# Kernel tuning notes

Hardware: AMD Instinct MI355X
Metric: run time of the kernel (lower is better)

Reference implementation:

```python
import jax, jax.numpy as jnp
import numpy as np

HID = 32
R = 3
B = 2
IN = 64
N = 100000
E = 1600000
G = 256


def setup_inputs() -> dict:
    key = jax.random.key(0)
    ks = jax.random.split(key, 16)
    x = jax.random.normal(ks[0], (N, IN), dtype=jnp.float32)
    src = jax.random.randint(ks[1], (E,), 0, N)
    dst = jax.random.randint(ks[2], (E,), 0, N)
    etype = jax.random.randint(ks[3], (E,), 0, R)
    graph_ids = jnp.sort(jax.random.randint(ks[4], (N,), 0, G))
    s = 0.05
    basis1 = jax.random.normal(ks[5], (B, IN, HID), dtype=jnp.float32) * s   # layer 1 basis
    basis_r = jax.random.normal(ks[6], (3, B, HID, HID), dtype=jnp.float32) * s  # layers 2-4
    w_comp = jax.random.normal(ks[7], (4, R, B), dtype=jnp.float32) * s     # per-layer basis coeffs
    loop1 = jax.random.normal(ks[8], (IN, HID), dtype=jnp.float32) * s
    loop_r = jax.random.normal(ks[9], (3, HID, HID), dtype=jnp.float32) * s
    bias = jnp.zeros((4, HID), dtype=jnp.float32)
    lin1_w = jax.random.normal(ks[10], (4 * HID, 64), dtype=jnp.float32) * s
    lin1_b = jnp.zeros((64,), dtype=jnp.float32)
    lin2_w = jax.random.normal(ks[11], (64, 1), dtype=jnp.float32) * s
    lin2_b = jnp.zeros((1,), dtype=jnp.float32)
    return dict(x=x, basis1=basis1, basis_r=basis_r, w_comp=w_comp, loop1=loop1,
                loop_r=loop_r, bias=bias, lin1_w=lin1_w, lin1_b=lin1_b,
                lin2_w=lin2_w, lin2_b=lin2_b, src=src, dst=dst, etype=etype,
                graph_ids=graph_ids, num_graphs=G)


def _rel_conv(h, basis, comp, loop_w, b, src, dst, etype, n_nodes):
    # basis-decomposed relation weights: W[r] = sum_b comp[r,b] * basis[b]
    W = jnp.einsum('rb,bio->rio', comp, basis)            # [R, in, out]
    h_rel = jnp.einsum('ni,rio->rno', h, W)               # [R, N, out]
    msg = h_rel[etype, src]                               # [E, out] edge-typed gather
    agg = jax.ops.segment_sum(msg, dst, num_segments=n_nodes)
    return agg + h @ loop_w + b                           # self-loop + bias


def reference(x, basis1, basis_r, w_comp, loop1, loop_r, bias,
              lin1_w, lin1_b, lin2_w, lin2_b,
              src, dst, etype, graph_ids, num_graphs):
    n = x.shape[0]
    h = jnp.tanh(_rel_conv(x, basis1, w_comp[0], loop1, bias[0], src, dst, etype, n))
    states = [h]
    for i in range(3):
        h = jnp.tanh(_rel_conv(h, basis_r[i], w_comp[i + 1], loop_r[i], bias[i + 1],
                               src, dst, etype, n))
        states.append(h)
    feat = jnp.concatenate(states, axis=1)                # [N, 128]
    # mean-pool nodes per graph (diff_pooling ~ dgl mean_nodes)
    summed = jax.ops.segment_sum(feat, graph_ids, num_segments=num_graphs)
    counts = jax.ops.segment_sum(jnp.ones((n,), feat.dtype), graph_ids,
                                 num_segments=num_graphs)
    pooled = summed / jnp.maximum(counts, 1.0)[:, None]   # [G, 128]
    hdn = jax.nn.relu(pooled @ lin1_w + lin1_b)
    out = jax.nn.sigmoid(hdn @ lin2_w + lin2_b)
    return out[:, 0]
```

## Files before the change

### kernel.cpp

```cpp
#include <hip/hip_runtime.h>
#include <cstdint>
#include <cmath>

#define DLO_BITS 7
#define DLO_MASK 127
#define CHUNK 4096

__global__ __launch_bounds__(256) void prep_w(
    const float* __restrict__ basis1,
    const float* __restrict__ w_comp,
    const float* __restrict__ loop1,
    float* __restrict__ W)
{
    int tid = blockIdx.x * 256 + threadIdx.x;
    if (tid < 8192) {
        int m = tid >> 11, io = tid & 2047;
        W[tid] = (m < 3)
            ? w_comp[m * 2] * basis1[io] + w_comp[m * 2 + 1] * basis1[2048 + io]
            : loop1[io];
    }
}

__global__ __launch_bounds__(256) void part_kernel(
    const int* __restrict__ src, const int* __restrict__ dst,
    const int* __restrict__ et, unsigned* __restrict__ eidx1,
    int* __restrict__ startTab,
    int* __restrict__ bcnt,
    int E, int NB)
{
    __shared__ unsigned rec[CHUNK];
    __shared__ int cnt[1024];
    __shared__ int w[1024];
    const int tid = threadIdx.x;
    const int base = blockIdx.x * CHUNK;
    int lim = E - base; if (lim > CHUNK) lim = CHUNK;

    cnt[tid] = 0; cnt[tid + 256] = 0; cnt[tid + 512] = 0; cnt[tid + 768] = 0;
    __syncthreads();
    for (int i = tid; i < lim; i += 256) {
        int e = base + i;
        int d = dst[e];
        rec[i] = (unsigned)src[e] | ((unsigned)et[e] << 17)
               | ((unsigned)(d & DLO_MASK) << 19);
        atomicAdd(&cnt[d >> DLO_BITS], 1);
    }
    __syncthreads();
    w[tid] = cnt[tid]; w[tid + 256] = cnt[tid + 256];
    w[tid + 512] = cnt[tid + 512]; w[tid + 768] = cnt[tid + 768];
    __syncthreads();
    for (int off = 1; off < 1024; off <<= 1) {
        int a0 = (tid >= off) ? w[tid - off] : 0;
        int a1 = (tid + 256 >= off) ? w[tid + 256 - off] : 0;
        int a2 = (tid + 512 >= off) ? w[tid + 512 - off] : 0;
        int a3 = w[tid + 768 - off];
        __syncthreads();
        w[tid] += a0; w[tid + 256] += a1; w[tid + 512] += a2; w[tid + 768] += a3;
        __syncthreads();
    }
    int* st = startTab + blockIdx.x * (NB + 1);
    for (int bk = tid; bk < NB; bk += 256) {
        int c = cnt[bk];
        int ex = w[bk] - c;
        st[bk] = base + ex;
        w[bk] = ex;
        if (c) atomicAdd(&bcnt[bk], c);
    }
    if (tid == 0) st[NB] = base + lim;
    __syncthreads();
    cnt[tid] = 0; cnt[tid + 256] = 0; cnt[tid + 512] = 0; cnt[tid + 768] = 0;
    __syncthreads();
    for (int i = tid; i < lim; i += 256) {
        int bk = dst[base + i] >> DLO_BITS;
        int pos = w[bk] + atomicAdd(&cnt[bk], 1);
        eidx1[base + pos] = rec[i];
    }
}

__global__ __launch_bounds__(1024) void scan_kernel(
    const int* __restrict__ bcnt, int* __restrict__ bbase, int NB)
{
    __shared__ int s[1024];
    int t = threadIdx.x;
    int v = (t < NB) ? bcnt[t] : 0;
    s[t] = v; __syncthreads();
    for (int off = 1; off < 1024; off <<= 1) {
        int u = (t >= off) ? s[t - off] : 0;
        __syncthreads();
        s[t] += u;
        __syncthreads();
    }
    if (t < NB) bbase[t] = s[t] - v;
}

__global__ __launch_bounds__(256) void bucket_sort_kernel(
    const unsigned* __restrict__ eidx1, const int* __restrict__ startTab,
    const int* __restrict__ bbase, unsigned* __restrict__ eidx2,
    int* __restrict__ rp, int* __restrict__ rend0, int* __restrict__ rend1,
    int* __restrict__ rend, int N, int NCH, int NB)
{
    __shared__ int rbase[512];
    __shared__ int racc[512];
    __shared__ int c512[512], excl[512], w2[512];
    const int tid = threadIdx.x, b = blockIdx.x;

    for (int j = tid; j < 512; j += 256) {
        int s = 0, len = 0;
        if (j < NCH) {
            s = startTab[j * (NB + 1) + b];
            len = startTab[j * (NB + 1) + b + 1] - s;
        }
        rbase[j] = s;
        racc[j] = len;
    }
    __syncthreads();
    for (int off = 1; off < 512; off <<= 1) {
        int a1 = (tid >= off) ? racc[tid - off] : 0;
        int a2 = (tid + 256 >= off) ? racc[tid + 256 - off] : 0;
        __syncthreads();
        racc[tid] += a1; racc[tid + 256] += a2;
        __syncthreads();
    }
    const int cnt = racc[NCH - 1];
    const int gbase = bbase[b];
    c512[tid] = 0; c512[tid + 256] = 0;
    __syncthreads();
    for (int i = tid; i < cnt; i += 256) {
        int lo = 0, hi = NCH - 1;
        while (lo < hi) { int mid = (lo + hi) >> 1; if (racc[mid] <= i) lo = mid + 1; else hi = mid; }
        unsigned pk = eidx1[rbase[lo] + (i - (lo ? racc[lo - 1] : 0))];
        int key = (((pk >> 19) & DLO_MASK) << 2) | ((pk >> 17) & 3);
        atomicAdd(&c512[key], 1);
    }
    __syncthreads();
    w2[tid] = c512[tid]; w2[tid + 256] = c512[tid + 256];
    __syncthreads();
    for (int off = 1; off < 512; off <<= 1) {
        int a1 = (tid >= off) ? w2[tid - off] : 0;
        int a2 = (tid + 256 >= off) ? w2[tid + 256 - off] : 0;
        __syncthreads();
        w2[tid] += a1; w2[tid + 256] += a2;
        __syncthreads();
    }
    excl[tid] = w2[tid] - c512[tid];
    excl[tid + 256] = w2[tid + 256] - c512[tid + 256];
    __syncthreads();
    if (tid < 128) {
        int n = (b << DLO_BITS) + tid;
        if (n < N) {
            int k0 = tid << 2;
            rp[n]    = gbase + excl[k0];
            rend0[n] = gbase + excl[k0 | 1];
            rend1[n] = gbase + excl[k0 | 2];
            rend[n]  = gbase + excl[k0 | 2] + c512[k0 | 2];
        }
    }
    __syncthreads();
    c512[tid] = 0; c512[tid + 256] = 0;
    __syncthreads();
    for (int i = tid; i < cnt; i += 256) {
        int lo = 0, hi = NCH - 1;
        while (lo < hi) { int mid = (lo + hi) >> 1; if (racc[mid] <= i) lo = mid + 1; else hi = mid; }
        unsigned pk = eidx1[rbase[lo] + (i - (lo ? racc[lo - 1] : 0))];
        int key = (((pk >> 19) & DLO_MASK) << 2) | ((pk >> 17) & 3);
        int p = excl[key] + atomicAdd(&c512[key], 1);
        eidx2[gbase + p] = pk;
    }
}

__global__ __launch_bounds__(256) void dense_kernel(
    const float* __restrict__ x,
    const float* __restrict__ W,
    const float* __restrict__ bias_l,
    float* __restrict__ hrel,
    float* __restrict__ agg,
    int N)
{
    __shared__ float sW[4 * 2048];
    __shared__ float sH[64 * 68];
    const int tid = threadIdx.x;
    for (int i = tid; i < 4 * 2048; i += 256) sW[i] = W[i];
    const int nb = blockIdx.x * 64;
    for (int idx = tid; idx < 64 * 64; idx += 256) {
        int n = idx >> 6, i = idx & 63;
        int gn = nb + n;
        sH[n * 68 + i] = (gn < N) ? x[(size_t)gn * 64 + i] : 0.0f;
    }
    __syncthreads();

    const int m  = tid >> 6;
    const int l  = tid & 63;
    const int ow = l & 7;
    const int ng = l >> 3;

    float acc[8][4];
    #pragma unroll
    for (int j = 0; j < 8; ++j)
        #pragma unroll
        for (int k = 0; k < 4; ++k) acc[j][k] = 0.0f;

    const float* wb = &sW[m * 2048 + ow * 4];
    #pragma unroll 2
    for (int i = 0; i < 64; i += 4) {
        float4 wv0 = *(const float4*)(wb + (i + 0) * 32);
        float4 wv1 = *(const float4*)(wb + (i + 1) * 32);
        float4 wv2 = *(const float4*)(wb + (i + 2) * 32);
        float4 wv3 = *(const float4*)(wb + (i + 3) * 32);
        #pragma unroll
        for (int j = 0; j < 8; ++j) {
            float4 hv = *(const float4*)&sH[(j * 8 + ng) * 68 + i];
            acc[j][0] += hv.x * wv0.x + hv.y * wv1.x + hv.z * wv2.x + hv.w * wv3.x;
            acc[j][1] += hv.x * wv0.y + hv.y * wv1.y + hv.z * wv2.y + hv.w * wv3.y;
            acc[j][2] += hv.x * wv0.z + hv.y * wv1.z + hv.z * wv2.z + hv.w * wv3.z;
            acc[j][3] += hv.x * wv0.w + hv.y * wv1.w + hv.z * wv2.w + hv.w * wv3.w;
        }
    }

    if (m < 3) {
        #pragma unroll
        for (int j = 0; j < 8; ++j) {
            int n = nb + j * 8 + ng;
            if (n < N)
                *(float4*)&hrel[((size_t)m * N + n) * 32 + ow * 4] =
                    make_float4(acc[j][0], acc[j][1], acc[j][2], acc[j][3]);
        }
    } else {
        float4 bb = *(const float4*)&bias_l[ow * 4];
        #pragma unroll
        for (int j = 0; j < 8; ++j) {
            int n = nb + j * 8 + ng;
            if (n < N)
                *(float4*)&agg[(size_t)n * 32 + ow * 4] =
                    make_float4(acc[j][0] + bb.x, acc[j][1] + bb.y,
                                acc[j][2] + bb.z, acc[j][3] + bb.w);
        }
    }
}

__global__ __launch_bounds__(256) void gather1_kernel(
    const unsigned* __restrict__ eidx, const int* __restrict__ rp,
    const int* __restrict__ rend0, const int* __restrict__ rend1,
    const int* __restrict__ rend,
    const float* __restrict__ hrel, const float* __restrict__ agg,
    float* __restrict__ feat, int N)
{
    int tid = blockIdx.x * 256 + threadIdx.x;
    int n = tid >> 3;
    if (n >= N) return;
    int c = (tid & 7) << 2;
    int e0 = rp[n], e1 = rend0[n], e2 = rend1[n], e3 = rend[n];
    const float4 bv = *(const float4*)&agg[(size_t)n * 32 + c];
    float ax = bv.x, ay = bv.y, az = bv.z, aw = bv.w;
    float bx = 0, by = 0, bz = 0, bw = 0;
    #pragma unroll
    for (int seg = 0; seg < 3; ++seg) {
        int ks = (seg == 0) ? e0 : ((seg == 1) ? e1 : e2);
        int ke = (seg == 0) ? e1 : ((seg == 1) ? e2 : e3);
        const float* hb = hrel + (size_t)seg * N * 32 + c;
        int k = ks;
        for (; k + 2 <= ke; k += 2) {
            unsigned p0 = eidx[k], p1 = eidx[k + 1];
            float4 v0 = *(const float4*)&hb[(size_t)(p0 & 0x1FFFF) * 32];
            float4 v1 = *(const float4*)&hb[(size_t)(p1 & 0x1FFFF) * 32];
            ax += v0.x; ay += v0.y; az += v0.z; aw += v0.w;
            bx += v1.x; by += v1.y; bz += v1.z; bw += v1.w;
        }
        if (k < ke) {
            unsigned p = eidx[k];
            float4 v = *(const float4*)&hb[(size_t)(p & 0x1FFFF) * 32];
            ax += v.x; ay += v.y; az += v.z; aw += v.w;
        }
    }
    float4* out = (float4*)&feat[(size_t)n * 128 + c];
    *out = make_float4(tanhf(ax + bx), tanhf(ay + by), tanhf(az + bz), tanhf(aw + bw));
}

__global__ __launch_bounds__(256) void fused_layer_kernel(
    const unsigned* __restrict__ eidx, const int* __restrict__ rp,
    const int* __restrict__ rend0, const int* __restrict__ rend1,
    const int* __restrict__ rend,
    const float* __restrict__ basis_b,
    const float* __restrict__ loop_w,
    const float* __restrict__ bias_l,
    const float* __restrict__ comp,
    const float* __restrict__ feat_in,
    float* __restrict__ feat_out,
    int N)
{
    __shared__ float sB0[1024], sB1[1024], sL[1024];
    __shared__ float sT0[32 * 36], sT1[32 * 36], sH[32 * 36];
    const int tid = threadIdx.x;
    for (int i = tid; i < 1024; i += 256) {
        sB0[i] = basis_b[i];
        sB1[i] = basis_b[1024 + i];
        sL[i]  = loop_w[i];
    }
    const int nn = tid >> 3, cg = (tid & 7) << 2;
    const int n = blockIdx.x * 32 + nn;

    float4 h4 = *(const float4*)&feat_in[(size_t)n * 128 + cg];
    *(float4*)&sH[nn * 36 + cg] = h4;

    int e0 = rp[n], e1 = rend0[n], e2 = rend1[n], e3 = rend[n];
    float t0x = 0, t0y = 0, t0z = 0, t0w = 0;
    float t1x = 0, t1y = 0, t1z = 0, t1w = 0;
    #pragma unroll
    for (int seg = 0; seg < 3; ++seg) {
        int ks = (seg == 0) ? e0 : ((seg == 1) ? e1 : e2);
        int ke = (seg == 0) ? e1 : ((seg == 1) ? e2 : e3);
        float sx = 0, sy = 0, sz = 0, sw = 0;
        float ux = 0, uy = 0, uz = 0, uw = 0;
        int k = ks;
        for (; k + 2 <= ke; k += 2) {
            unsigned p0 = eidx[k], p1 = eidx[k + 1];
            float4 v0 = *(const float4*)&feat_in[(size_t)(p0 & 0x1FFFF) * 128 + cg];
            float4 v1 = *(const float4*)&feat_in[(size_t)(p1 & 0x1FFFF) * 128 + cg];
            sx += v0.x; sy += v0.y; sz += v0.z; sw += v0.w;
            ux += v1.x; uy += v1.y; uz += v1.z; uw += v1.w;
        }
        if (k < ke) {
            unsigned p = eidx[k];
            float4 v = *(const float4*)&feat_in[(size_t)(p & 0x1FFFF) * 128 + cg];
            sx += v.x; sy += v.y; sz += v.z; sw += v.w;
        }
        sx += ux; sy += uy; sz += uz; sw += uw;
        float c0 = comp[seg * 2], c1 = comp[seg * 2 + 1];
        t0x += c0 * sx; t0y += c0 * sy; t0z += c0 * sz; t0w += c0 * sw;
        t1x += c1 * sx; t1y += c1 * sy; t1z += c1 * sz; t1w += c1 * sw;
    }
    *(float4*)&sT0[nn * 36 + cg] = make_float4(t0x, t0y, t0z, t0w);
    *(float4*)&sT1[nn * 36 + cg] = make_float4(t1x, t1y, t1z, t1w);
    __syncthreads();

    float4 bb = *(const float4*)&bias_l[cg];
    float a[4] = {bb.x, bb.y, bb.z, bb.w};
    #pragma unroll 8
    for (int kk = 0; kk < 32; ++kk) {
        float p0 = sT0[nn * 36 + kk];
        float p1 = sT1[nn * 36 + kk];
        float hh = sH[nn * 36 + kk];
        float4 b0 = *(const float4*)&sB0[kk * 32 + cg];
        float4 b1 = *(const float4*)&sB1[kk * 32 + cg];
        float4 lw = *(const float4*)&sL[kk * 32 + cg];
        a[0] += p0 * b0.x + p1 * b1.x + hh * lw.x;
        a[1] += p0 * b0.y + p1 * b1.y + hh * lw.y;
        a[2] += p0 * b0.z + p1 * b1.z + hh * lw.z;
        a[3] += p0 * b0.w + p1 * b1.w + hh * lw.w;
    }
    *(float4*)&feat_out[(size_t)n * 128 + cg] =
        make_float4(tanhf(a[0]), tanhf(a[1]), tanhf(a[2]), tanhf(a[3]));
}

__global__ __launch_bounds__(256) void pool_kernel(
    const float* __restrict__ feat, const int* __restrict__ gid,
    float* __restrict__ pooled, float* __restrict__ cntArr, int N)
{
    int chunk0 = blockIdx.x * 128;
    int ch = threadIdx.x & 127, half = threadIdx.x >> 7;
    int n = chunk0 + half;
    int lim = chunk0 + 128; if (lim > N) lim = N;
    if (n >= lim) return;
    int cur = gid[n];
    float acc = 0.0f; int cc = 0;
    for (; n < lim; n += 2) {
        int g = gid[n];
        if (g != cur) {
            atomicAdd(&pooled[(size_t)cur * 128 + ch], acc);
            if (ch == 0) atomicAdd(&cntArr[cur], (float)cc);
            acc = 0.0f; cc = 0; cur = g;
        }
        acc += feat[(size_t)n * 128 + ch];
        ++cc;
    }
    atomicAdd(&pooled[(size_t)cur * 128 + ch], acc);
    if (ch == 0) atomicAdd(&cntArr[cur], (float)cc);
}

__global__ __launch_bounds__(64) void mlp_kernel(
    const float* __restrict__ pooled, const float* __restrict__ cntArr,
    const float* __restrict__ w1, const float* __restrict__ b1,
    const float* __restrict__ w2, const float* __restrict__ b2,
    float* __restrict__ out)
{
    int g = blockIdx.x;
    int t = threadIdx.x;
    float inv = 1.0f / fmaxf(cntArr[g], 1.0f);
    float acc = b1[t];
    #pragma unroll 8
    for (int k = 0; k < 128; ++k)
        acc += pooled[(size_t)g * 128 + k] * inv * w1[k * 64 + t];
    float h = fmaxf(acc, 0.0f);
    float p = h * w2[t];
    #pragma unroll
    for (int off = 32; off > 0; off >>= 1) p += __shfl_down(p, off, 64);
    if (t == 0) out[g] = 1.0f / (1.0f + expf(-(p + b2[0])));
}

extern "C" void kernel_launch(void* const* d_in, const int* in_sizes, int n_in,
                              void* d_out, int out_size, void* d_ws, size_t ws_size,
                              hipStream_t stream)
{
    const float* x       = (const float*)d_in[0];
    const float* basis1  = (const float*)d_in[1];
    const float* basis_r = (const float*)d_in[2];
    const float* w_comp  = (const float*)d_in[3];
    const float* loop1   = (const float*)d_in[4];
    const float* loop_r  = (const float*)d_in[5];
    const float* bias    = (const float*)d_in[6];
    const float* lin1_w  = (const float*)d_in[7];
    const float* lin1_b  = (const float*)d_in[8];
    const float* lin2_w  = (const float*)d_in[9];
    const float* lin2_b  = (const float*)d_in[10];
    const int*   src     = (const int*)d_in[11];
    const int*   dst     = (const int*)d_in[12];
    const int*   etype   = (const int*)d_in[13];
    const int*   gid     = (const int*)d_in[14];

    const int N = in_sizes[0] / 64;
    const int E = in_sizes[11];
    const int G = out_size;
    const int NB = (N + DLO_MASK) >> DLO_BITS;
    const int NCH = (E + CHUNK - 1) / CHUNK;

    float* ws      = (float*)d_ws;
    float* W       = ws;
    float* hrel    = W + 8192;
    float* agg     = hrel + (size_t)3 * N * 32;
    float* feat    = agg + (size_t)N * 32;
    float* pooled  = feat + (size_t)N * 128;
    float* cntArr  = pooled + (size_t)G * 128;
    int*   bcnt    = (int*)(cntArr + G);
    int*   bbase   = bcnt + NB;
    int*   rp      = bbase + NB;
    int*   rend0   = rp + N;
    int*   rend1   = rend0 + N;
    int*   rend    = rend1 + N;
    unsigned* eidx2 = (unsigned*)(rend + N);
    unsigned* eidx1 = (unsigned*)feat;
    int* startTab  = (int*)feat + (size_t)NCH * CHUNK;

    hipMemsetAsync(pooled, 0, ((size_t)G * 128 + G + NB) * sizeof(float), stream);
    prep_w<<<32, 256, 0, stream>>>(basis1, w_comp, loop1, W);

    part_kernel<<<NCH, 256, 0, stream>>>(src, dst, etype, eidx1, startTab, bcnt, E, NB);
    scan_kernel<<<1, 1024, 0, stream>>>(bcnt, bbase, NB);
    bucket_sort_kernel<<<NB, 256, 0, stream>>>(eidx1, startTab, bbase, eidx2,
                                               rp, rend0, rend1, rend, N, NCH, NB);

    dense_kernel<<<(N + 63) / 64, 256, 0, stream>>>(x, W, bias, hrel, agg, N);
    gather1_kernel<<<(N * 8 + 255) / 256, 256, 0, stream>>>(
        eidx2, rp, rend0, rend1, rend, hrel, agg, feat, N);

    for (int l = 1; l < 4; ++l) {
        fused_layer_kernel<<<(N + 31) / 32, 256, 0, stream>>>(
            eidx2, rp, rend0, rend1, rend,
            basis_r + (size_t)(l - 1) * 2048,
            loop_r + (size_t)(l - 1) * 1024,
            bias + l * 32,
            w_comp + l * 6,
            feat + (l - 1) * 32,
            feat + l * 32,
            N);
    }

    pool_kernel<<<(N + 127) / 128, 256, 0, stream>>>(feat, gid, pooled, cntArr, N);
    mlp_kernel<<<G, 64, 0, stream>>>(pooled, cntArr, lin1_w, lin1_b, lin2_w, lin2_b, (float*)d_out);
}
```

Measured before the change: 324.6 us.

## Drop shared staging; read dense weights from global and shuffle per-node vectors

The dense kernel no longer copies the 32KB weight matrix into shared memory and instead reads the weights straight from global or L2 memory. This cuts LDS use per block and should allow more resident blocks. The fused layer kernel replaces its shared-memory staging of the aggregated and self features with wavefront shuffles (__shfl) among the 8 lanes that own a node. This removes three shared tiles and one barrier, though a barrier is still needed after loading the basis weights. The costs are global-load latency for the weights and extra shuffle instructions.

```diff
diff --git a/kernel.cpp b/kernel.cpp
--- a/kernel.cpp
+++ b/kernel.cpp
@@ -175,10 +175,8 @@
     float* __restrict__ agg,
     int N)
 {
-    __shared__ float sW[4 * 2048];
     __shared__ float sH[64 * 68];
     const int tid = threadIdx.x;
-    for (int i = tid; i < 4 * 2048; i += 256) sW[i] = W[i];
     const int nb = blockIdx.x * 64;
     for (int idx = tid; idx < 64 * 64; idx += 256) {
         int n = idx >> 6, i = idx & 63;
@@ -198,7 +196,7 @@
         #pragma unroll
         for (int k = 0; k < 4; ++k) acc[j][k] = 0.0f;
 
-    const float* wb = &sW[m * 2048 + ow * 4];
+    const float* wb = W + m * 2048 + ow * 4;
     #pragma unroll 2
     for (int i = 0; i < 64; i += 4) {
         float4 wv0 = *(const float4*)(wb + (i + 0) * 32);
@@ -287,22 +285,21 @@
     int N)
 {
     __shared__ float sB0[1024], sB1[1024], sL[1024];
-    __shared__ float sT0[32 * 36], sT1[32 * 36], sH[32 * 36];
     const int tid = threadIdx.x;
     for (int i = tid; i < 1024; i += 256) {
         sB0[i] = basis_b[i];
         sB1[i] = basis_b[1024 + i];
         sL[i]  = loop_w[i];
     }
+    __syncthreads();
+
     const int nn = tid >> 3, cg = (tid & 7) << 2;
     const int n = blockIdx.x * 32 + nn;
 
     float4 h4 = *(const float4*)&feat_in[(size_t)n * 128 + cg];
-    *(float4*)&sH[nn * 36 + cg] = h4;
 
     int e0 = rp[n], e1 = rend0[n], e2 = rend1[n], e3 = rend[n];
-    float t0x = 0, t0y = 0, t0z = 0, t0w = 0;
-    float t1x = 0, t1y = 0, t1z = 0, t1w = 0;
+    float t0[4] = {0, 0, 0, 0}, t1[4] = {0, 0, 0, 0};
     #pragma unroll
     for (int seg = 0; seg < 3; ++seg) {
         int ks = (seg == 0) ? e0 : ((seg == 1) ? e1 : e2);
@@ -324,30 +321,34 @@
         }
         sx += ux; sy += uy; sz += uz; sw += uw;
         float c0 = comp[seg * 2], c1 = comp[seg * 2 + 1];
-        t0x += c0 * sx; t0y += c0 * sy; t0z += c0 * sz; t0w += c0 * sw;
-        t1x += c1 * sx; t1y += c1 * sy; t1z += c1 * sz; t1w += c1 * sw;
-    }
-    *(float4*)&sT0[nn * 36 + cg] = make_float4(t0x, t0y, t0z, t0w);
-    *(float4*)&sT1[nn * 36 + cg] = make_float4(t1x, t1y, t1z, t1w);
-    __syncthreads();
-
+        t0[0] += c0 * sx; t0[1] += c0 * sy; t0[2] += c0 * sz; t0[3] += c0 * sw;
+        t1[0] += c1 * sx; t1[1] += c1 * sy; t1[2] += c1 * sz; t1[3] += c1 * sw;
+    }
+
+    float hreg[4] = {h4.x, h4.y, h4.z, h4.w};
     float4 bb = *(const float4*)&bias_l[cg];
-    float a[4] = {bb.x, bb.y, bb.z, bb.w};
-    #pragma unroll 8
-    for (int kk = 0; kk < 32; ++kk) {
-        float p0 = sT0[nn * 36 + kk];
-        float p1 = sT1[nn * 36 + kk];
-        float hh = sH[nn * 36 + kk];
-        float4 b0 = *(const float4*)&sB0[kk * 32 + cg];
-        float4 b1 = *(const float4*)&sB1[kk * 32 + cg];
-        float4 lw = *(const float4*)&sL[kk * 32 + cg];
-        a[0] += p0 * b0.x + p1 * b1.x + hh * lw.x;
-        a[1] += p0 * b0.y + p1 * b1.y + hh * lw.y;
-        a[2] += p0 * b0.z + p1 * b1.z + hh * lw.z;
-        a[3] += p0 * b0.w + p1 * b1.w + hh * lw.w;
+    float a0 = bb.x, a1 = bb.y, a2 = bb.z, a3 = bb.w;
+    const int lbase = (tid & 63) & ~7;
+    #pragma unroll
+    for (int q = 0; q < 8; ++q) {
+        const int sl = lbase + q;
+        #pragma unroll
+        for (int r = 0; r < 4; ++r) {
+            const int kk = q * 4 + r;
+            float p0 = __shfl(t0[r], sl, 64);
+            float p1 = __shfl(t1[r], sl, 64);
+            float hh = __shfl(hreg[r], sl, 64);
+            float4 b0 = *(const float4*)&sB0[kk * 32 + cg];
+            float4 b1 = *(const float4*)&sB1[kk * 32 + cg];
+            float4 lw = *(const float4*)&sL[kk * 32 + cg];
+            a0 += p0 * b0.x + p1 * b1.x + hh * lw.x;
+            a1 += p0 * b0.y + p1 * b1.y + hh * lw.y;
+            a2 += p0 * b0.z + p1 * b1.z + hh * lw.z;
+            a3 += p0 * b0.w + p1 * b1.w + hh * lw.w;
+        }
     }
     *(float4*)&feat_out[(size_t)n * 128 + cg] =
-        make_float4(tanhf(a[0]), tanhf(a[1]), tanhf(a[2]), tanhf(a[3]));
+        make_float4(tanhf(a0), tanhf(a1), tanhf(a2), tanhf(a3));
 }
 
 __global__ __launch_bounds__(256) void pool_kernel(
```

New measurement: 658.1 us. 103% more time.
